# Performance work log

Measured on AMD Instinct MI355X. Metric: run time of the kernel, lower is better.

The kernel has to match this reference:

```python
import jax, jax.numpy as jnp
import numpy as np
from jax import lax

LAMBDA_KL = 0.3
CLAMP_EPS = 1e-6
COS_EPS = 1e-8


def setup_inputs() -> dict:
    key = jax.random.key(0)
    k1, k2, k3, k4, k5, k6 = jax.random.split(key, 6)
    B, Cf, Cp, S = 8, 32, 4, 64
    L = 32  # overlap length (cur_end - cur_start == adj_end - adj_start)
    sf = jax.random.normal(k1, (B, Cf, S, S, S), dtype=jnp.float32)
    tf = jax.random.normal(k2, (B, Cf, S, S, S), dtype=jnp.float32)
    sp = jax.random.uniform(k3, (B, Cp, S, S, S), dtype=jnp.float32)
    tp = jax.random.uniform(k4, (B, Cp, S, S, S), dtype=jnp.float32)
    cur_start = jax.random.randint(k5, (B,), 0, S - L + 1, dtype=jnp.int32)
    adj_start = jax.random.randint(k6, (B,), 0, S - L + 1, dtype=jnp.int32)
    return {
        "sf": sf, "tf": tf, "sp": sp, "tp": tp,
        "cur_start": cur_start, "adj_start": adj_start,
        "axis": 0, "overlap_len": L, "full_size": S,
    }


def reference(sf, tf, sp, tp, cur_start, adj_start, axis, overlap_len, full_size):
    # axis/overlap_len/full_size are static Python ints.
    L = int(overlap_len)
    ax = int(axis)
    feat = sf.shape[ax + 2]          # feature size along sliced axis
    r = feat // int(full_size)       # _feat_bounds ratio (exact here: feat == full_size)
    flen = max(1, L * r)             # constant feature slice length

    def per_sample(sf_b, tf_b, sp_b, tp_b, cs, a_s):
        # sp_b/tp_b: [Cp, D, H, W]; sf_b/tf_b: [Cf, D, H, W]
        sps = lax.dynamic_slice_in_dim(jnp.clip(sp_b, CLAMP_EPS, 1.0 - CLAMP_EPS), cs, L, axis=ax + 1)
        tps = lax.dynamic_slice_in_dim(jnp.clip(tp_b, CLAMP_EPS, 1.0 - CLAMP_EPS), a_s, L, axis=ax + 1)
        # F.kl_div(log(sp), tp, reduction='batchmean') with leading batch dim of 1
        kl = jnp.sum(tps * (jnp.log(tps) - jnp.log(sps)))
        # feature bounds: fs = floor(s*feat/full), fe = ceil(e*feat/full) -> starts scale by r
        sfs = lax.dynamic_slice_in_dim(sf_b, cs * r, flen, axis=ax + 1)
        tfs = lax.dynamic_slice_in_dim(tf_b, a_s * r, flen, axis=ax + 1)
        Cf = sf_b.shape[0]
        sfl = sfs.reshape(Cf, -1)   # flatten(2) of [1, Cf, ...]
        tfl = tfs.reshape(Cf, -1)
        # cosine similarity over channel dim (dim=1 in torch after unsqueeze)
        num = jnp.sum(sfl * tfl, axis=0)
        den = (jnp.maximum(jnp.linalg.norm(sfl, axis=0), COS_EPS)
               * jnp.maximum(jnp.linalg.norm(tfl, axis=0), COS_EPS))
        cos = 1.0 - jnp.mean(num / den)
        return cos + LAMBDA_KL * kl

    losses = jax.vmap(per_sample)(sf, tf, sp, tp, cur_start, adj_start)
    return jnp.mean(losses)
```

## Files before the change

kernel.cpp:

```cpp
#include <hip/hip_runtime.h>

namespace {

constexpr int kB  = 8;
constexpr int kCF = 32;
constexpr int kCP = 4;
constexpr int kS  = 64;
constexpr int kL  = 32;
constexpr int kPlane = kS * kS;
constexpr long long kChStride = (long long)kS * kPlane;
constexpr int kMCos = kL * kPlane;
constexpr int kCosBlocksPerB = kMCos / (256 * 4);
constexpr int kKlElems = kCP * kL * kPlane;
constexpr int kKlBlocksPerB = kKlElems / (256 * 8);
constexpr int kGridCos = kB * kCosBlocksPerB;
constexpr int kGridKl  = kB * kKlBlocksPerB;
constexpr int kGridTotal = kGridCos + kGridKl;
constexpr float kClampEps = 1e-6f;
constexpr float kCosEps = 1e-8f;

typedef float floatx4 __attribute__((ext_vector_type(4)));

__device__ __forceinline__ floatx4 nt_load4(const float* p) {
  return __builtin_nontemporal_load(reinterpret_cast<const floatx4*>(p));
}

__device__ __forceinline__ float block_reduce_sum(float v) {
  #pragma unroll
  for (int off = 32; off > 0; off >>= 1) v += __shfl_down(v, off, 64);
  __shared__ float smem[4];
  const int lane = threadIdx.x & 63;
  const int wid  = threadIdx.x >> 6;
  if (lane == 0) smem[wid] = v;
  __syncthreads();
  float r = 0.f;
  if (threadIdx.x == 0) r = smem[0] + smem[1] + smem[2] + smem[3];
  __syncthreads();
  return r;
}

__device__ __forceinline__ float kl_term(float sv, float tv) {
  const float sc = fminf(fmaxf(sv, kClampEps), 1.f - kClampEps);
  const float tc = fminf(fmaxf(tv, kClampEps), 1.f - kClampEps);
  return tc * (__logf(tc) - __logf(sc));
}

__global__ __launch_bounds__(256) void fused_main(
    const float* __restrict__ sf, const float* __restrict__ tf,
    const float* __restrict__ sp, const float* __restrict__ tp,
    const int* __restrict__ cur_start, const int* __restrict__ adj_start,
    float* __restrict__ partial) {
  const int blk = blockIdx.x;
  float local = 0.f;

  if (blk < kGridCos) {
    const int b     = blk >> 7;
    const int chunk = blk & (kCosBlocksPerB - 1);
    const int cs = cur_start[b];
    const int as = adj_start[b];
    const int pos = chunk * 1024 + (int)threadIdx.x * 4;
    const int dd  = pos >> 12;
    const int rem = pos & (kPlane - 1);
    const float* sptr = sf + ((long long)b * kCF * kS + (cs + dd)) * kPlane + rem;
    const float* tptr = tf + ((long long)b * kCF * kS + (as + dd)) * kPlane + rem;

    floatx4 dot = {0.f, 0.f, 0.f, 0.f};
    floatx4 na  = {0.f, 0.f, 0.f, 0.f};
    floatx4 nb  = {0.f, 0.f, 0.f, 0.f};
    #pragma unroll 8
    for (int c = 0; c < kCF; ++c) {
      const floatx4 a = nt_load4(sptr + c * kChStride);
      const floatx4 t = nt_load4(tptr + c * kChStride);
      dot += a * t;
      na  += a * a;
      nb  += t * t;
    }
    local =
        dot.x / (fmaxf(sqrtf(na.x), kCosEps) * fmaxf(sqrtf(nb.x), kCosEps)) +
        dot.y / (fmaxf(sqrtf(na.y), kCosEps) * fmaxf(sqrtf(nb.y), kCosEps)) +
        dot.z / (fmaxf(sqrtf(na.z), kCosEps) * fmaxf(sqrtf(nb.z), kCosEps)) +
        dot.w / (fmaxf(sqrtf(na.w), kCosEps) * fmaxf(sqrtf(nb.w), kCosEps));
  } else {
    const int kblk  = blk - kGridCos;
    const int b     = kblk >> 8;
    const int chunk = kblk & (kKlBlocksPerB - 1);
    const int cs = cur_start[b];
    const int as = adj_start[b];
    const int base = chunk * 2048;
    #pragma unroll
    for (int half = 0; half < 2; ++half) {
      const int pos = base + half * 1024 + (int)threadIdx.x * 4;
      const int c   = pos >> 17;
      const int m   = pos & (kMCos - 1);
      const int dd  = m >> 12;
      const int rem = m & (kPlane - 1);
      const floatx4 s4 = nt_load4(
          sp + ((long long)(b * kCP + c) * kS + (cs + dd)) * kPlane + rem);
      const floatx4 t4 = nt_load4(
          tp + ((long long)(b * kCP + c) * kS + (as + dd)) * kPlane + rem);
      local += kl_term(s4.x, t4.x) + kl_term(s4.y, t4.y) +
               kl_term(s4.z, t4.z) + kl_term(s4.w, t4.w);
    }
  }

  const float s = block_reduce_sum(local);
  if (threadIdx.x == 0) partial[blk] = s;
}

__global__ __launch_bounds__(256) void final_kernel(
    const float* __restrict__ partial, float* __restrict__ out) {
  float cosAcc = 0.f, klAcc = 0.f;
  for (int i = threadIdx.x; i < kGridCos; i += 256) cosAcc += partial[i];
  for (int i = kGridCos + (int)threadIdx.x; i < kGridTotal; i += 256)
    klAcc += partial[i];
  const float cosTot = block_reduce_sum(cosAcc);
  const float klTot  = block_reduce_sum(klAcc);
  if (threadIdx.x == 0) {
    out[0] = 1.f - cosTot / (float)(kB * kMCos) + 0.3f * klTot / (float)kB;
  }
}

}

extern "C" void kernel_launch(void* const* d_in, const int* in_sizes, int n_in,
                              void* d_out, int out_size, void* d_ws, size_t ws_size,
                              hipStream_t stream) {
  const float* sf = (const float*)d_in[0];
  const float* tf = (const float*)d_in[1];
  const float* sp = (const float*)d_in[2];
  const float* tp = (const float*)d_in[3];
  const int* cur_start = (const int*)d_in[4];
  const int* adj_start = (const int*)d_in[5];
  float* out = (float*)d_out;
  float* partial = (float*)d_ws;

  fused_main<<<kGridTotal, 256, 0, stream>>>(
      sf, tf, sp, tp, cur_start, adj_start, partial);
  final_kernel<<<1, 256, 0, stream>>>(partial, out);
}
```

Measured before the change: 56.53 us.

## Merge cosine and KL work into every block for uniform load balance

Every block now does both a slice of the cosine-similarity work (2 floats per thread across 32 channels) and a slice of the KL work, replacing the old split where separate blocks handled each branch. This removes branch divergence between block types and evens out per-block memory traffic. Scaling is folded in before the block reduction, so the final kernel sums one combined array. The cosine loads narrow from 16-byte to 8-byte vectors, which may lower per-load efficiency.

```diff
diff --git a/kernel.cpp b/kernel.cpp
--- a/kernel.cpp
+++ b/kernel.cpp
@@ -10,17 +10,20 @@
 constexpr int kPlane = kS * kS;
 constexpr long long kChStride = (long long)kS * kPlane;
 constexpr int kMCos = kL * kPlane;
-constexpr int kCosBlocksPerB = kMCos / (256 * 4);
 constexpr int kKlElems = kCP * kL * kPlane;
-constexpr int kKlBlocksPerB = kKlElems / (256 * 8);
-constexpr int kGridCos = kB * kCosBlocksPerB;
-constexpr int kGridKl  = kB * kKlBlocksPerB;
-constexpr int kGridTotal = kGridCos + kGridKl;
+constexpr int kGrid = 2048;
+constexpr int kBlocksPerB = kGrid / kB;
 constexpr float kClampEps = 1e-6f;
 constexpr float kCosEps = 1e-8f;
+constexpr float kCosScale = 1.0f / (float)((long long)kB * kMCos);
+constexpr float kKlScale  = 0.3f / (float)kB;
 
+typedef float floatx2 __attribute__((ext_vector_type(2)));
 typedef float floatx4 __attribute__((ext_vector_type(4)));
 
+__device__ __forceinline__ floatx2 nt_load2(const float* p) {
+  return __builtin_nontemporal_load(reinterpret_cast<const floatx2*>(p));
+}
 __device__ __forceinline__ floatx4 nt_load4(const float* p) {
   return __builtin_nontemporal_load(reinterpret_cast<const floatx4*>(p));
 }
@@ -51,73 +54,64 @@
     const int* __restrict__ cur_start, const int* __restrict__ adj_start,
     float* __restrict__ partial) {
   const int blk = blockIdx.x;
-  float local = 0.f;
+  const int b   = blk >> 8;
+  const int i   = blk & (kBlocksPerB - 1);
+  const int cs  = cur_start[b];
+  const int as  = adj_start[b];
 
-  if (blk < kGridCos) {
-    const int b     = blk >> 7;
-    const int chunk = blk & (kCosBlocksPerB - 1);
-    const int cs = cur_start[b];
-    const int as = adj_start[b];
-    const int pos = chunk * 1024 + (int)threadIdx.x * 4;
-    const int dd  = pos >> 12;
-    const int rem = pos & (kPlane - 1);
-    const float* sptr = sf + ((long long)b * kCF * kS + (cs + dd)) * kPlane + rem;
-    const float* tptr = tf + ((long long)b * kCF * kS + (as + dd)) * kPlane + rem;
-
-    floatx4 dot = {0.f, 0.f, 0.f, 0.f};
-    floatx4 na  = {0.f, 0.f, 0.f, 0.f};
-    floatx4 nb  = {0.f, 0.f, 0.f, 0.f};
+  float cosLocal;
+  {
+    const int posbase = i << 9;
+    const int dd  = posbase >> 12;
+    const int rem = (posbase & (kPlane - 1)) + (int)threadIdx.x * 2;
+    const float* s0 = sf + ((long long)b * kCF * kS + (cs + dd)) * kPlane + rem;
+    const float* t0 = tf + ((long long)b * kCF * kS + (as + dd)) * kPlane + rem;
+    floatx2 dot = {0.f, 0.f};
+    floatx2 na  = {0.f, 0.f};
+    floatx2 nb  = {0.f, 0.f};
     #pragma unroll 8
     for (int c = 0; c < kCF; ++c) {
-      const floatx4 a = nt_load4(sptr + c * kChStride);
-      const floatx4 t = nt_load4(tptr + c * kChStride);
+      const floatx2 a = nt_load2(s0 + c * kChStride);
+      const floatx2 t = nt_load2(t0 + c * kChStride);
       dot += a * t;
       na  += a * a;
       nb  += t * t;
     }
-    local =
+    cosLocal =
         dot.x / (fmaxf(sqrtf(na.x), kCosEps) * fmaxf(sqrtf(nb.x), kCosEps)) +
-        dot.y / (fmaxf(sqrtf(na.y), kCosEps) * fmaxf(sqrtf(nb.y), kCosEps)) +
-        dot.z / (fmaxf(sqrtf(na.z), kCosEps) * fmaxf(sqrtf(nb.z), kCosEps)) +
-        dot.w / (fmaxf(sqrtf(na.w), kCosEps) * fmaxf(sqrtf(nb.w), kCosEps));
-  } else {
-    const int kblk  = blk - kGridCos;
-    const int b     = kblk >> 8;
-    const int chunk = kblk & (kKlBlocksPerB - 1);
-    const int cs = cur_start[b];
-    const int as = adj_start[b];
-    const int base = chunk * 2048;
+        dot.y / (fmaxf(sqrtf(na.y), kCosEps) * fmaxf(sqrtf(nb.y), kCosEps));
+  }
+
+  float klLocal = 0.f;
+  {
+    const int fbase = i << 11;
+    const int c   = fbase >> 17;
+    const int m   = fbase & (kMCos - 1);
+    const int ddk = m >> 12;
+    const int remk = m & (kPlane - 1);
+    const float* sb = sp + ((long long)(b * kCP + c) * kS + (cs + ddk)) * kPlane + remk;
+    const float* tb = tp + ((long long)(b * kCP + c) * kS + (as + ddk)) * kPlane + remk;
     #pragma unroll
-    for (int half = 0; half < 2; ++half) {
-      const int pos = base + half * 1024 + (int)threadIdx.x * 4;
-      const int c   = pos >> 17;
-      const int m   = pos & (kMCos - 1);
-      const int dd  = m >> 12;
-      const int rem = m & (kPlane - 1);
-      const floatx4 s4 = nt_load4(
-          sp + ((long long)(b * kCP + c) * kS + (cs + dd)) * kPlane + rem);
-      const floatx4 t4 = nt_load4(
-          tp + ((long long)(b * kCP + c) * kS + (as + dd)) * kPlane + rem);
-      local += kl_term(s4.x, t4.x) + kl_term(s4.y, t4.y) +
-               kl_term(s4.z, t4.z) + kl_term(s4.w, t4.w);
+    for (int h = 0; h < 2; ++h) {
+      const int off = h * 1024 + (int)threadIdx.x * 4;
+      const floatx4 s4 = nt_load4(sb + off);
+      const floatx4 t4 = nt_load4(tb + off);
+      klLocal += kl_term(s4.x, t4.x) + kl_term(s4.y, t4.y) +
+                 kl_term(s4.z, t4.z) + kl_term(s4.w, t4.w);
     }
   }
 
+  const float local = -cosLocal * kCosScale + klLocal * kKlScale;
   const float s = block_reduce_sum(local);
   if (threadIdx.x == 0) partial[blk] = s;
 }
 
 __global__ __launch_bounds__(256) void final_kernel(
     const float* __restrict__ partial, float* __restrict__ out) {
-  float cosAcc = 0.f, klAcc = 0.f;
-  for (int i = threadIdx.x; i < kGridCos; i += 256) cosAcc += partial[i];
-  for (int i = kGridCos + (int)threadIdx.x; i < kGridTotal; i += 256)
-    klAcc += partial[i];
-  const float cosTot = block_reduce_sum(cosAcc);
-  const float klTot  = block_reduce_sum(klAcc);
-  if (threadIdx.x == 0) {
-    out[0] = 1.f - cosTot / (float)(kB * kMCos) + 0.3f * klTot / (float)kB;
-  }
+  float acc = 0.f;
+  for (int i = threadIdx.x; i < kGrid; i += 256) acc += partial[i];
+  const float tot = block_reduce_sum(acc);
+  if (threadIdx.x == 0) out[0] = 1.f + tot;
 }
 
 }
@@ -134,7 +128,7 @@
   float* out = (float*)d_out;
   float* partial = (float*)d_ws;
 
-  fused_main<<<kGridTotal, 256, 0, stream>>>(
+  fused_main<<<kGrid, 256, 0, stream>>>(
       sf, tf, sp, tp, cur_start, adj_start, partial);
   final_kernel<<<1, 256, 0, stream>>>(partial, out);
 }
```

New measurement: 53.42 us. 1.06x faster.
